# Kernel tuning notes

Hardware: AMD Instinct MI355X
Metric: run time of the kernel (lower is better)

Reference implementation:

```python
import jax, jax.numpy as jnp
import numpy as np

N, D = 8192, 64


def setup_inputs() -> dict:
    key = jax.random.key(0)
    k1, k2, k3 = jax.random.split(key, 3)
    X = jax.random.normal(k1, (N, D), dtype=jnp.float32)
    target = jax.random.normal(k2, (N,), dtype=jnp.float32)
    params = jax.random.uniform(k3, (D,), dtype=jnp.float32)  # positive ARD weights
    return {"X": X, "target": target, "params": params}


def reference(X, target, params):
    # ARD-RBF kernel: k(x, y) = exp(-sum(params * (x - y)^2))
    # = exp(-||xs - ys||^2) with xs = x * sqrt(params)
    Xs = X * jnp.sqrt(params)  # [N, D]
    sq = jnp.sum(Xs * Xs, axis=-1)  # [N]
    d2 = jnp.maximum(sq[:, None] + sq[None, :] - 2.0 * (Xs @ Xs.T), 0.0)  # [N, N]
    K = jnp.exp(-d2)
    # torch version initializes K = eye(N) and never overwrites the diagonal
    n = X.shape[0]
    K = K.at[jnp.arange(n), jnp.arange(n)].set(1.0)
    K_target = jnp.outer(target, target)  # [N, N]
    kta = jnp.sum(K * K_target) / (n * jnp.sqrt(jnp.sum(K * K)))
    return -kta
```

## Files before the change

### kernel.cpp

```cpp
#include <hip/hip_runtime.h>
#include <hip/hip_bf16.h>

#define NROWS 8192
#define DIM 64
#define NT 64
#define NTRI (NT * (NT + 1) / 2)

typedef __attribute__((ext_vector_type(8))) short short8;
typedef __attribute__((ext_vector_type(4))) float f32x4;

static constexpr float LOG2E = 1.4426950408889634f;

#if defined(__has_builtin) && __has_builtin(__builtin_amdgcn_exp2f)
#define EXP2F(x) __builtin_amdgcn_exp2f(x)
#else
#define EXP2F(x) exp2f(x)
#endif

__global__ __launch_bounds__(256) void prep_kernel(const float* __restrict__ X,
                                                   const float* __restrict__ params,
                                                   float* __restrict__ Lsq,
                                                   short* __restrict__ Xp) {
    int tid  = threadIdx.x;
    int wave = tid >> 6, lane = tid & 63;
    int r8 = lane >> 3, c = lane & 7;
    int row = blockIdx.x * 32 + wave * 8 + r8;

    const float* xr = X + row * DIM + c * 8;
    float4 x0 = *(const float4*)xr;
    float4 x1 = *(const float4*)(xr + 4);
    float4 p0 = *(const float4*)(params + c * 8);
    float4 p1 = *(const float4*)(params + c * 8 + 4);

    float v[8];
    v[0] = x0.x * sqrtf(p0.x); v[1] = x0.y * sqrtf(p0.y);
    v[2] = x0.z * sqrtf(p0.z); v[3] = x0.w * sqrtf(p0.w);
    v[4] = x1.x * sqrtf(p1.x); v[5] = x1.y * sqrtf(p1.y);
    v[6] = x1.z * sqrtf(p1.z); v[7] = x1.w * sqrtf(p1.w);

    short8 h;
    float s = 0.f;
    #pragma unroll
    for (int i = 0; i < 8; ++i) {
        __hip_bfloat16 b = __float2bfloat16(v[i]);
        union { __hip_bfloat16 bb; short ss; } u; u.bb = b;
        h[i] = u.ss;
        float bf = __bfloat162float(b);
        s += bf * bf;
    }

    int panel = row >> 4, pr = row & 15;
    ((short8*)Xp)[panel * 128 + c * 16 + pr] = h;

    #pragma unroll
    for (int m = 1; m < 8; m <<= 1) s += __shfl_xor(s, m, 64);
    if (c == 0) Lsq[row] = LOG2E * s;
}

__global__ __launch_bounds__(256) void kta_main(const short* __restrict__ Xp,
                                                const float* __restrict__ Lsq,
                                                const float* __restrict__ t,
                                                float2* __restrict__ partial) {
    int k = blockIdx.x;
    int it = (int)((129.0f - sqrtf(16641.0f - 8.0f * (float)k)) * 0.5f);
    if (it > NT - 1) it = NT - 1;
    while ((it * (129 - it)) / 2 > k) --it;
    while (((it + 1) * (128 - it)) / 2 <= k) ++it;
    int jt = it + (k - (it * (129 - it)) / 2);

    int tid  = threadIdx.x;
    int wave = tid >> 6, lane = tid & 63;
    int quad = lane >> 4, l16 = lane & 15;
    int rbase = it * 128 + (wave >> 1) * 64;
    int cbase = jt * 128 + (wave & 1) * 64;

    const short8* Xpv = (const short8*)Xp;
    int pA0 = rbase >> 4, pB0 = cbase >> 4;
    short8 afr[4][2], bfr[4][2];
    #pragma unroll
    for (int rt = 0; rt < 4; ++rt) {
        #pragma unroll
        for (int kc = 0; kc < 2; ++kc) {
            afr[rt][kc] = Xpv[(pA0 + rt) * 128 + (kc * 4 + quad) * 16 + l16];
            bfr[rt][kc] = Xpv[(pB0 + rt) * 128 + (kc * 4 + quad) * 16 + l16];
        }
    }

    f32x4 c[4][4];
    #pragma unroll
    for (int rt = 0; rt < 4; ++rt)
        #pragma unroll
        for (int ct = 0; ct < 4; ++ct)
            c[rt][ct] = (f32x4){0.f, 0.f, 0.f, 0.f};

    #pragma unroll
    for (int rt = 0; rt < 4; ++rt)
        #pragma unroll
        for (int ct = 0; ct < 4; ++ct) {
            c[rt][ct] = __builtin_amdgcn_mfma_f32_16x16x32_bf16(afr[rt][0], bfr[ct][0], c[rt][ct], 0, 0, 0);
            c[rt][ct] = __builtin_amdgcn_mfma_f32_16x16x32_bf16(afr[rt][1], bfr[ct][1], c[rt][ct], 0, 0, 0);
        }

    float LsqR[4][4], tR[4][4];
    #pragma unroll
    for (int rt = 0; rt < 4; ++rt)
        #pragma unroll
        for (int r = 0; r < 4; ++r) {
            int row = rbase + rt * 16 + quad * 4 + r;
            LsqR[rt][r] = Lsq[row];
            tR[rt][r]   = t[row];
        }
    float LsqC[4], tC[4];
    #pragma unroll
    for (int ct = 0; ct < 4; ++ct) {
        int col = cbase + ct * 16 + l16;
        LsqC[ct] = Lsq[col];
        tC[ct]   = t[col];
    }

    bool diagwave = (it == jt) && ((wave >> 1) == (wave & 1));
    int col_l = cbase + l16;

    float s1 = 0.f, s2 = 0.f;
    #pragma unroll
    for (int rt = 0; rt < 4; ++rt)
        #pragma unroll
        for (int r = 0; r < 4; ++r) {
            int row = rbase + rt * 16 + quad * 4 + r;
            float nr = LsqR[rt][r];
            float s1row = 0.f;
            #pragma unroll
            for (int ct = 0; ct < 4; ++ct) {
                float dot = c[rt][ct][r];
                float K = EXP2F(fmaf(dot, 2.0f * LOG2E, -(nr + LsqC[ct])));
                if (diagwave && (row == (col_l + ct * 16)))
                    K = 1.0f;
                s1row = fmaf(K, tC[ct], s1row);
                s2    = fmaf(K, K, s2);
            }
            s1 = fmaf(s1row, tR[rt][r], s1);
        }

    float w = (it == jt) ? 1.0f : 2.0f;
    s1 *= w; s2 *= w;
    #pragma unroll
    for (int m = 32; m > 0; m >>= 1) {
        s1 += __shfl_xor(s1, m, 64);
        s2 += __shfl_xor(s2, m, 64);
    }

    __shared__ float2 red[4];
    if (lane == 0) red[wave] = make_float2(s1, s2);
    __syncthreads();
    if (tid == 0) {
        float2 a = red[0], b = red[1], cc = red[2], d = red[3];
        partial[k] = make_float2(a.x + b.x + cc.x + d.x, a.y + b.y + cc.y + d.y);
    }
}

__global__ __launch_bounds__(256) void finalize_kernel(const float2* __restrict__ partial,
                                                       float* __restrict__ out) {
    float s1 = 0.f, s2 = 0.f;
    for (int i = threadIdx.x; i < NTRI; i += 256) {
        float2 p = partial[i];
        s1 += p.x;
        s2 += p.y;
    }
    #pragma unroll
    for (int m = 32; m > 0; m >>= 1) {
        s1 += __shfl_xor(s1, m, 64);
        s2 += __shfl_xor(s2, m, 64);
    }
    __shared__ float r1[4], r2[4];
    int wave = threadIdx.x >> 6, lane = threadIdx.x & 63;
    if (lane == 0) { r1[wave] = s1; r2[wave] = s2; }
    __syncthreads();
    if (threadIdx.x == 0) {
        float a = r1[0] + r1[1] + r1[2] + r1[3];
        float b = r2[0] + r2[1] + r2[2] + r2[3];
        out[0] = -a / ((float)NROWS * sqrtf(b));
    }
}

extern "C" void kernel_launch(void* const* d_in, const int* in_sizes, int n_in,
                              void* d_out, int out_size, void* d_ws, size_t ws_size,
                              hipStream_t stream) {
    const float* X      = (const float*)d_in[0];
    const float* target = (const float*)d_in[1];
    const float* params = (const float*)d_in[2];
    float* out = (float*)d_out;

    float* ws = (float*)d_ws;
    float2* partial = (float2*)ws;
    float* Lsq = ws + 8192;
    short* Xp  = (short*)(ws + 16384);

    prep_kernel<<<NROWS / 32, 256, 0, stream>>>(X, params, Lsq, Xp);
    kta_main<<<NTRI, 256, 0, stream>>>(Xp, Lsq, target, partial);
    finalize_kernel<<<1, 256, 0, stream>>>(partial, out);
}
```

Baseline: 74.19 us.

## Fuse prep, main and finalize into one persistent cooperative kernel

Merges the three launches into a single cooperative kernel. Grid-wide syncs separate the prep phase, a persistent grid-stride loop over the 2080 triangle tiles (512 blocks), and a final reduction in block 0. Row norms and targets are packed into one float2 array so each row needs a single load, and the explicit diagonal K=1 override is dropped on the assumption that the computed diagonal already evaluates to about one. This removes launch gaps and the large partial array, at the cost of two grid barriers, fewer blocks to hide memory latency, and a small numerical deviation on the diagonal.

```diff
diff --git a/kernel.cpp b/kernel.cpp
--- a/kernel.cpp
+++ b/kernel.cpp
@@ -1,10 +1,14 @@
 #include <hip/hip_runtime.h>
 #include <hip/hip_bf16.h>
+#include <hip/hip_cooperative_groups.h>
+
+namespace cg = cooperative_groups;
 
 #define NROWS 8192
 #define DIM 64
 #define NT 64
 #define NTRI (NT * (NT + 1) / 2)
+#define GRID 512
 
 typedef __attribute__((ext_vector_type(8))) short short8;
 typedef __attribute__((ext_vector_type(4))) float f32x4;
@@ -17,168 +21,153 @@
 #define EXP2F(x) exp2f(x)
 #endif
 
-__global__ __launch_bounds__(256) void prep_kernel(const float* __restrict__ X,
-                                                   const float* __restrict__ params,
-                                                   float* __restrict__ Lsq,
-                                                   short* __restrict__ Xp) {
-    int tid  = threadIdx.x;
+__global__ __launch_bounds__(256, 2) void kta_fused(
+    const float* __restrict__ X, const float* __restrict__ params,
+    const float* __restrict__ t, float2* __restrict__ Lt,
+    short* __restrict__ Xp, float2* __restrict__ partial,
+    float* __restrict__ out) {
+    cg::grid_group gg = cg::this_grid();
+    int tid = threadIdx.x, bid = blockIdx.x;
     int wave = tid >> 6, lane = tid & 63;
-    int r8 = lane >> 3, c = lane & 7;
-    int row = blockIdx.x * 32 + wave * 8 + r8;
 
-    const float* xr = X + row * DIM + c * 8;
-    float4 x0 = *(const float4*)xr;
-    float4 x1 = *(const float4*)(xr + 4);
-    float4 p0 = *(const float4*)(params + c * 8);
-    float4 p1 = *(const float4*)(params + c * 8 + 4);
+    if (wave < 2) {
+        int r8 = lane >> 3, c = lane & 7;
+        int row = bid * 16 + wave * 8 + r8;
+        const float* xr = X + row * DIM + c * 8;
+        float4 x0 = *(const float4*)xr;
+        float4 x1 = *(const float4*)(xr + 4);
+        float4 p0 = *(const float4*)(params + c * 8);
+        float4 p1 = *(const float4*)(params + c * 8 + 4);
 
-    float v[8];
-    v[0] = x0.x * sqrtf(p0.x); v[1] = x0.y * sqrtf(p0.y);
-    v[2] = x0.z * sqrtf(p0.z); v[3] = x0.w * sqrtf(p0.w);
-    v[4] = x1.x * sqrtf(p1.x); v[5] = x1.y * sqrtf(p1.y);
-    v[6] = x1.z * sqrtf(p1.z); v[7] = x1.w * sqrtf(p1.w);
+        float v[8];
+        v[0] = x0.x * sqrtf(p0.x); v[1] = x0.y * sqrtf(p0.y);
+        v[2] = x0.z * sqrtf(p0.z); v[3] = x0.w * sqrtf(p0.w);
+        v[4] = x1.x * sqrtf(p1.x); v[5] = x1.y * sqrtf(p1.y);
+        v[6] = x1.z * sqrtf(p1.z); v[7] = x1.w * sqrtf(p1.w);
 
-    short8 h;
-    float s = 0.f;
-    #pragma unroll
-    for (int i = 0; i < 8; ++i) {
-        __hip_bfloat16 b = __float2bfloat16(v[i]);
-        union { __hip_bfloat16 bb; short ss; } u; u.bb = b;
-        h[i] = u.ss;
-        float bf = __bfloat162float(b);
-        s += bf * bf;
+        short8 h;
+        float s = 0.f;
+        #pragma unroll
+        for (int i = 0; i < 8; ++i) {
+            __hip_bfloat16 b = __float2bfloat16(v[i]);
+            union { __hip_bfloat16 bb; short ss; } u; u.bb = b;
+            h[i] = u.ss;
+            float bf = __bfloat162float(b);
+            s += bf * bf;
+        }
+        int panel = row >> 4, pr = row & 15;
+        ((short8*)Xp)[panel * 128 + c * 16 + pr] = h;
+        #pragma unroll
+        for (int m = 1; m < 8; m <<= 1) s += __shfl_xor(s, m, 64);
+        if (c == 0) Lt[row] = make_float2(LOG2E * s, t[row]);
+    }
+    gg.sync();
+
+    int quad = lane >> 4, l16 = lane & 15;
+    const short8* Xpv = (const short8*)Xp;
+    float s1 = 0.f, s2 = 0.f;
+
+    for (int k = bid; k < NTRI; k += GRID) {
+        int it = (int)((129.0f - sqrtf(16641.0f - 8.0f * (float)k)) * 0.5f);
+        if (it > NT - 1) it = NT - 1;
+        while ((it * (129 - it)) / 2 > k) --it;
+        while (((it + 1) * (128 - it)) / 2 <= k) ++it;
+        int jt = it + (k - (it * (129 - it)) / 2);
+
+        int rbase = it * 128 + (wave >> 1) * 64;
+        int cbase = jt * 128 + (wave & 1) * 64;
+        int pA0 = rbase >> 4, pB0 = cbase >> 4;
+
+        short8 afr[4][2], bfr[4][2];
+        #pragma unroll
+        for (int rt = 0; rt < 4; ++rt) {
+            #pragma unroll
+            for (int kc = 0; kc < 2; ++kc) {
+                afr[rt][kc] = Xpv[(pA0 + rt) * 128 + (kc * 4 + quad) * 16 + l16];
+                bfr[rt][kc] = Xpv[(pB0 + rt) * 128 + (kc * 4 + quad) * 16 + l16];
+            }
+        }
+
+        f32x4 c[4][4];
+        #pragma unroll
+        for (int rt = 0; rt < 4; ++rt)
+            #pragma unroll
+            for (int ct = 0; ct < 4; ++ct)
+                c[rt][ct] = (f32x4){0.f, 0.f, 0.f, 0.f};
+
+        #pragma unroll
+        for (int rt = 0; rt < 4; ++rt)
+            #pragma unroll
+            for (int ct = 0; ct < 4; ++ct) {
+                c[rt][ct] = __builtin_amdgcn_mfma_f32_16x16x32_bf16(afr[rt][0], bfr[ct][0], c[rt][ct], 0, 0, 0);
+                c[rt][ct] = __builtin_amdgcn_mfma_f32_16x16x32_bf16(afr[rt][1], bfr[ct][1], c[rt][ct], 0, 0, 0);
+            }
+
+        float2 LtR[4][4];
+        #pragma unroll
+        for (int rt = 0; rt < 4; ++rt)
+            #pragma unroll
+            for (int r = 0; r < 4; ++r)
+                LtR[rt][r] = Lt[rbase + rt * 16 + quad * 4 + r];
+        float2 LtC[4];
+        #pragma unroll
+        for (int ct = 0; ct < 4; ++ct)
+            LtC[ct] = Lt[cbase + ct * 16 + l16];
+
+        float ts1 = 0.f, ts2 = 0.f;
+        #pragma unroll
+        for (int rt = 0; rt < 4; ++rt)
+            #pragma unroll
+            for (int r = 0; r < 4; ++r) {
+                float nr = LtR[rt][r].x;
+                float s1row = 0.f;
+                #pragma unroll
+                for (int ct = 0; ct < 4; ++ct) {
+                    float K = EXP2F(fmaf(c[rt][ct][r], 2.0f * LOG2E, -(nr + LtC[ct].x)));
+                    s1row = fmaf(K, LtC[ct].y, s1row);
+                    ts2   = fmaf(K, K, ts2);
+                }
+                ts1 = fmaf(s1row, LtR[rt][r].y, ts1);
+            }
+
+        float w = (it == jt) ? 1.0f : 2.0f;
+        s1 = fmaf(ts1, w, s1);
+        s2 = fmaf(ts2, w, s2);
     }
 
-    int panel = row >> 4, pr = row & 15;
-    ((short8*)Xp)[panel * 128 + c * 16 + pr] = h;
-
-    #pragma unroll
-    for (int m = 1; m < 8; m <<= 1) s += __shfl_xor(s, m, 64);
-    if (c == 0) Lsq[row] = LOG2E * s;
-}
-
-__global__ __launch_bounds__(256) void kta_main(const short* __restrict__ Xp,
-                                                const float* __restrict__ Lsq,
-                                                const float* __restrict__ t,
-                                                float2* __restrict__ partial) {
-    int k = blockIdx.x;
-    int it = (int)((129.0f - sqrtf(16641.0f - 8.0f * (float)k)) * 0.5f);
-    if (it > NT - 1) it = NT - 1;
-    while ((it * (129 - it)) / 2 > k) --it;
-    while (((it + 1) * (128 - it)) / 2 <= k) ++it;
-    int jt = it + (k - (it * (129 - it)) / 2);
-
-    int tid  = threadIdx.x;
-    int wave = tid >> 6, lane = tid & 63;
-    int quad = lane >> 4, l16 = lane & 15;
-    int rbase = it * 128 + (wave >> 1) * 64;
-    int cbase = jt * 128 + (wave & 1) * 64;
-
-    const short8* Xpv = (const short8*)Xp;
-    int pA0 = rbase >> 4, pB0 = cbase >> 4;
-    short8 afr[4][2], bfr[4][2];
-    #pragma unroll
-    for (int rt = 0; rt < 4; ++rt) {
-        #pragma unroll
-        for (int kc = 0; kc < 2; ++kc) {
-            afr[rt][kc] = Xpv[(pA0 + rt) * 128 + (kc * 4 + quad) * 16 + l16];
-            bfr[rt][kc] = Xpv[(pB0 + rt) * 128 + (kc * 4 + quad) * 16 + l16];
-        }
-    }
-
-    f32x4 c[4][4];
-    #pragma unroll
-    for (int rt = 0; rt < 4; ++rt)
-        #pragma unroll
-        for (int ct = 0; ct < 4; ++ct)
-            c[rt][ct] = (f32x4){0.f, 0.f, 0.f, 0.f};
-
-    #pragma unroll
-    for (int rt = 0; rt < 4; ++rt)
-        #pragma unroll
-        for (int ct = 0; ct < 4; ++ct) {
-            c[rt][ct] = __builtin_amdgcn_mfma_f32_16x16x32_bf16(afr[rt][0], bfr[ct][0], c[rt][ct], 0, 0, 0);
-            c[rt][ct] = __builtin_amdgcn_mfma_f32_16x16x32_bf16(afr[rt][1], bfr[ct][1], c[rt][ct], 0, 0, 0);
-        }
-
-    float LsqR[4][4], tR[4][4];
-    #pragma unroll
-    for (int rt = 0; rt < 4; ++rt)
-        #pragma unroll
-        for (int r = 0; r < 4; ++r) {
-            int row = rbase + rt * 16 + quad * 4 + r;
-            LsqR[rt][r] = Lsq[row];
-            tR[rt][r]   = t[row];
-        }
-    float LsqC[4], tC[4];
-    #pragma unroll
-    for (int ct = 0; ct < 4; ++ct) {
-        int col = cbase + ct * 16 + l16;
-        LsqC[ct] = Lsq[col];
-        tC[ct]   = t[col];
-    }
-
-    bool diagwave = (it == jt) && ((wave >> 1) == (wave & 1));
-    int col_l = cbase + l16;
-
-    float s1 = 0.f, s2 = 0.f;
-    #pragma unroll
-    for (int rt = 0; rt < 4; ++rt)
-        #pragma unroll
-        for (int r = 0; r < 4; ++r) {
-            int row = rbase + rt * 16 + quad * 4 + r;
-            float nr = LsqR[rt][r];
-            float s1row = 0.f;
-            #pragma unroll
-            for (int ct = 0; ct < 4; ++ct) {
-                float dot = c[rt][ct][r];
-                float K = EXP2F(fmaf(dot, 2.0f * LOG2E, -(nr + LsqC[ct])));
-                if (diagwave && (row == (col_l + ct * 16)))
-                    K = 1.0f;
-                s1row = fmaf(K, tC[ct], s1row);
-                s2    = fmaf(K, K, s2);
-            }
-            s1 = fmaf(s1row, tR[rt][r], s1);
-        }
-
-    float w = (it == jt) ? 1.0f : 2.0f;
-    s1 *= w; s2 *= w;
     #pragma unroll
     for (int m = 32; m > 0; m >>= 1) {
         s1 += __shfl_xor(s1, m, 64);
         s2 += __shfl_xor(s2, m, 64);
     }
-
     __shared__ float2 red[4];
     if (lane == 0) red[wave] = make_float2(s1, s2);
     __syncthreads();
     if (tid == 0) {
         float2 a = red[0], b = red[1], cc = red[2], d = red[3];
-        partial[k] = make_float2(a.x + b.x + cc.x + d.x, a.y + b.y + cc.y + d.y);
+        partial[bid] = make_float2(a.x + b.x + cc.x + d.x, a.y + b.y + cc.y + d.y);
     }
-}
+    gg.sync();
 
-__global__ __launch_bounds__(256) void finalize_kernel(const float2* __restrict__ partial,
-                                                       float* __restrict__ out) {
-    float s1 = 0.f, s2 = 0.f;
-    for (int i = threadIdx.x; i < NTRI; i += 256) {
-        float2 p = partial[i];
-        s1 += p.x;
-        s2 += p.y;
-    }
-    #pragma unroll
-    for (int m = 32; m > 0; m >>= 1) {
-        s1 += __shfl_xor(s1, m, 64);
-        s2 += __shfl_xor(s2, m, 64);
-    }
-    __shared__ float r1[4], r2[4];
-    int wave = threadIdx.x >> 6, lane = threadIdx.x & 63;
-    if (lane == 0) { r1[wave] = s1; r2[wave] = s2; }
-    __syncthreads();
-    if (threadIdx.x == 0) {
-        float a = r1[0] + r1[1] + r1[2] + r1[3];
-        float b = r2[0] + r2[1] + r2[2] + r2[3];
-        out[0] = -a / ((float)NROWS * sqrtf(b));
+    if (bid == 0) {
+        float a = 0.f, b = 0.f;
+        for (int i = tid; i < GRID; i += 256) {
+            float2 p = partial[i];
+            a += p.x; b += p.y;
+        }
+        #pragma unroll
+        for (int m = 32; m > 0; m >>= 1) {
+            a += __shfl_xor(a, m, 64);
+            b += __shfl_xor(b, m, 64);
+        }
+        __shared__ float r1[4], r2[4];
+        if (lane == 0) { r1[wave] = a; r2[wave] = b; }
+        __syncthreads();
+        if (tid == 0) {
+            float fa = r1[0] + r1[1] + r1[2] + r1[3];
+            float fb = r2[0] + r2[1] + r2[2] + r2[3];
+            out[0] = -fa / ((float)NROWS * sqrtf(fb));
+        }
     }
 }
 
@@ -192,10 +181,11 @@
 
     float* ws = (float*)d_ws;
     float2* partial = (float2*)ws;
-    float* Lsq = ws + 8192;
-    short* Xp  = (short*)(ws + 16384);
+    float2* Lt = (float2*)(ws + 2048);
+    short*  Xp = (short*)(ws + 2048 + 16384);
 
-    prep_kernel<<<NROWS / 32, 256, 0, stream>>>(X, params, Lsq, Xp);
-    kta_main<<<NTRI, 256, 0, stream>>>(Xp, Lsq, target, partial);
-    finalize_kernel<<<1, 256, 0, stream>>>(partial, out);
+    void* args[] = {(void*)&X, (void*)&params, (void*)&target,
+                    (void*)&Lt, (void*)&Xp, (void*)&partial, (void*)&out};
+    hipLaunchCooperativeKernel((const void*)kta_fused, dim3(GRID), dim3(256),
+                               args, 0, stream);
 }
```

Result: slower. 174.2 us (+134.8%).
